# Performance work log

Hardware: AMD Instinct MI355X
Metric: run time of the kernel (lower is better)

Reference implementation:

```python
import jax, jax.numpy as jnp
import numpy as np

B, NIN, NH, SUB, HID = 8192, 1433, 64, 6, 128
TEMP, LAMB, ITERS = 0.4, 20.0, 5

def prelu(x, a):
    return jnp.where(x >= 0, x, a * x)

def l2norm(x):
    # F.normalize with eps clamp
    n = jnp.maximum(jnp.linalg.norm(x, axis=-1, keepdims=True), 1e-12)
    return x / n

def setup_inputs() -> dict:
    key = jax.random.key(0)
    ks = jax.random.split(key, 16)
    inp = {}
    inp['seq1'] = jax.random.normal(ks[0], (B, SUB, NIN), jnp.float32)
    inp['seq2'] = jax.random.normal(ks[1], (B, SUB, NIN), jnp.float32)
    inp['adj1'] = jax.random.uniform(ks[2], (B, SUB, SUB), jnp.float32)
    inp['adj2'] = jax.random.uniform(ks[3], (B, SUB, SUB), jnp.float32)
    inp['rescale_ratio'] = jax.random.uniform(ks[4], (B, SUB - 1, SUB - 1), jnp.float32)
    inp['gcn_W'] = jax.random.normal(ks[5], (NH, NIN), jnp.float32) / np.sqrt(NIN)
    inp['gcn_b'] = jnp.zeros((NH,), jnp.float32)
    inp['gcn_a'] = jnp.float32(0.25)
    inp['dec_W1'] = jax.random.normal(ks[6], (HID, NH * 4), jnp.float32) / np.sqrt(NH * 4)
    inp['dec_b1'] = jnp.zeros((HID,), jnp.float32)
    inp['dec_a1'] = jnp.float32(0.25)
    inp['dec_W2'] = jax.random.normal(ks[7], (HID, HID), jnp.float32) / np.sqrt(HID)
    inp['dec_b2'] = jnp.zeros((HID,), jnp.float32)
    inp['dec_a2'] = jnp.float32(0.25)
    inp['dec_W3'] = jax.random.normal(ks[8], (NIN, HID), jnp.float32) / np.sqrt(HID)
    inp['dec_b3'] = jnp.zeros((NIN,), jnp.float32)
    inp['dec_a3'] = jnp.float32(0.25)
    inp['disc_W'] = jax.random.normal(ks[9], (1, NH, NH), jnp.float32) / np.sqrt(NH)
    inp['disc_b'] = jnp.zeros((1,), jnp.float32)
    inp['subgraph_size'] = 4
    return inp

def sinkhorn_score(g1, n1, g2, n2, rescale_ratio):
    # cost has grad; transport is computed under no_grad in torch
    cost = (1.0 - jnp.einsum('bik,bjk->bij', l2norm(g1), l2norm(g2))) * rescale_ratio
    sg = jax.lax.stop_gradient
    g1s, n1s, g2s, n2s, costs = sg(g1), sg(n1), sg(g2), sg(n2), sg(cost)
    r = jnp.einsum('bik,bjk->bij', g1s, n2s)            # [B, N, 1]
    r = jnp.where(r <= 0, 1e-8, r)
    r = r / jnp.sum(r, axis=1, keepdims=True)
    c = jnp.einsum('bik,bjk->bij', g2s, n1s)            # [B, N, 1]
    c = jnp.where(c <= 0, 1e-8, c)
    c = c / jnp.sum(c, axis=1, keepdims=True)
    P = jnp.exp(-LAMB * costs)                          # [B, N, N]
    u = jnp.ones_like(c) / c.shape[1]
    for _ in range(ITERS):
        v = r / jnp.einsum('bij,bjk->bik', P, u)
        u = c / jnp.einsum('bji,bjk->bik', P, v)
    # diag(v) @ P @ diag(u)
    transport = v * P * jnp.swapaxes(u, 1, 2)           # [B, N, N]
    S = jnp.sum(transport * (1.0 - cost), axis=(1, 2))[:, None]  # [B, 1]
    return S

def reference(seq1, seq2, adj1, adj2, rescale_ratio, gcn_W, gcn_b, gcn_a,
              dec_W1, dec_b1, dec_a1, dec_W2, dec_b2, dec_a2, dec_W3, dec_b3, dec_a3,
              disc_W, disc_b, subgraph_size):
    def gcn(seq, adj):
        fts = jnp.einsum('bnf,hf->bnh', seq, gcn_W)
        return prelu(jnp.einsum('bnm,bmh->bnh', adj, fts) + gcn_b, gcn_a)
    h1 = gcn(seq1, adj1)   # [B, SUB, NH]
    h2 = gcn(seq2, adj2)
    # swap last two rows, then split graph-part / node-part
    def swap(h):
        return jnp.concatenate([h[:, :-2], h[:, -1:], h[:, -2:-1]], axis=1)
    h1n, h2n = swap(h1), swap(h2)
    g1, n1 = h1n[:, :-1], h1n[:, -1:]
    g2, n2 = h2n[:, :-1], h2n[:, -1:]
    S = sinkhorn_score(g1, n1, g2, n2, rescale_ratio)
    loss_pos = jnp.exp(S / TEMP) * 2.0                  # [B, 1]
    # decoder (subgraph_size=4 path): sub_node = h[:, :sub_size-2, :]
    x = h1[:, :subgraph_size, :].reshape(h1.shape[0], -1)
    x = prelu(x @ dec_W1.T + dec_b1, dec_a1)
    x = prelu(x @ dec_W2.T + dec_b2, dec_a2)
    node_recons = prelu(x @ dec_W3.T + dec_b3, dec_a3)  # [B, NIN]
    # discriminator (avg readout over context nodes, bilinear score)
    c = jnp.mean(h1[:, :-1, :], axis=1)                 # [B, NH]
    hp = h1[:, -1, :]                                   # [B, NH]
    s1 = jnp.einsum('bi,oij,bj->bo', hp, disc_W, c) + disc_b
    c_mi = jnp.concatenate([c[-2:-1], c[:-1]], axis=0)  # negsamp_round=1 shift
    s2 = jnp.einsum('bi,oij,bj->bo', hp, disc_W, c_mi) + disc_b
    logits = jnp.concatenate([s1, s2], axis=1)          # [B, 2]
    return jnp.concatenate([loss_pos, node_recons, logits], axis=1)  # [B, 1+NIN+2]
```

## Files before the change

kernel.cpp:

```cpp
#include <hip/hip_runtime.h>
#include <math.h>

#define BB   8192
#define NIN  1433
#define NH   64
#define SUBG 6
#define HID  128

typedef __attribute__((ext_vector_type(8))) short bf16x8;
typedef __attribute__((ext_vector_type(4))) float f32x4;
typedef __attribute__((ext_vector_type(16))) float f32x16;

__device__ __forceinline__ short f2bf(float x) {
  unsigned u = __float_as_uint(x);
  unsigned r = (u + 0x7fffu + ((u >> 16) & 1u)) >> 16;
  return (short)r;
}
__device__ __forceinline__ float bf2f(short s) {
  return __uint_as_float(((unsigned)(unsigned short)s) << 16);
}
__device__ __forceinline__ float allred64(float v) {
#pragma unroll
  for (int m = 1; m < 64; m <<= 1) v += __shfl_xor(v, m, 64);
  return v;
}

__device__ __forceinline__ void gload_lds16(const short* g, short* l) {
  __builtin_amdgcn_global_load_lds(
      (const __attribute__((address_space(1))) void*)g,
      (__attribute__((address_space(3))) void*)l, 16, 0, 0);
}

#define WAITV(N)                                            \
  {                                                         \
    asm volatile("s_waitcnt vmcnt(" #N ")" ::: "memory");   \
    __builtin_amdgcn_sched_barrier(0);                      \
  }
#define BARRIER()                                           \
  {                                                         \
    __builtin_amdgcn_s_barrier();                           \
    __builtin_amdgcn_sched_barrier(0);                      \
  }

__device__ __forceinline__ void pack16_impl(const float* __restrict__ src,
                                            short* __restrict__ hi, short* __restrict__ lo,
                                            int Oreal, int NF, int Kreal, int idx) {
  int j    = idx & 7;
  int lane = (idx >> 3) & 63;
  int nf   = (idx >> 9) % NF;
  int c    = idx / (NF * 512);
  int o = nf * 16 + (lane & 15);
  int k = c * 32 + ((lane >> 4) << 3) + j;
  float v = (o < Oreal && k < Kreal) ? src[(size_t)o * Kreal + k] : 0.f;
  short h = f2bf(v);
  hi[idx] = h;
  lo[idx] = f2bf(v - bf2f(h));
}

__device__ __forceinline__ void pack32_impl(const float* __restrict__ src,
                                            short* __restrict__ hi, short* __restrict__ lo,
                                            int idx) {
  int j    = idx & 7;
  int lane = (idx >> 3) & 63;
  int s    = (idx >> 9) & 3;
  int c    = idx >> 11;
  int o = (s & 1) * 32 + (lane & 31);
  int k = c * 32 + ((s >> 1) << 4) + ((lane >> 5) << 3) + j;
  float v = (k < NIN) ? src[(size_t)o * NIN + k] : 0.f;
  short h = f2bf(v);
  hi[idx] = h;
  lo[idx] = f2bf(v - bf2f(h));
}

#define PK_G  (45 * 4 * 512)
#define PK_B1 (8 * 8 * 512)
#define PK_B2 (4 * 8 * 512)
#define PK_B3 (4 * 90 * 512)
#define PK_TOTAL (PK_G + PK_B1 + PK_B2 + PK_B3)

__global__ void pack_all(const float* __restrict__ gcnW, const float* __restrict__ W1,
                         const float* __restrict__ W2, const float* __restrict__ W3,
                         short* Gh, short* Gl, short* B1h, short* B1l,
                         short* B2h, short* B2l, short* B3h, short* B3l) {
  int idx = blockIdx.x * 256 + threadIdx.x;
  if (idx < PK_G) { pack32_impl(gcnW, Gh, Gl, idx); return; }
  idx -= PK_G;
  if (idx < PK_B1) { pack16_impl(W1, B1h, B1l, 128, 8, 256, idx); return; }
  idx -= PK_B1;
  if (idx < PK_B2) { pack16_impl(W2, B2h, B2l, 128, 8, 128, idx); return; }
  idx -= PK_B2;
  if (idx < PK_B3) { pack16_impl(W3, B3h, B3l, 1433, 90, 128, idx); }
}

__global__ __launch_bounds__(384, 3) void gcn_mfma(
    const float* __restrict__ seq1, const float* __restrict__ seq2,
    const short* __restrict__ Gh, const short* __restrict__ Gl,
    float* __restrict__ fts1, float* __restrict__ fts2)
{
  __shared__ short sB[4][4096];
  const int tid = threadIdx.x;
  const int sid = blockIdx.x >> 8;
  const int bb  = blockIdx.x & 255;
  const float* __restrict__ seq = sid ? seq2 : seq1;
  float* __restrict__ fout = sid ? fts2 : fts1;
  const int w = tid >> 6, lane = tid & 63;
  const int l31 = lane & 31, lg2 = lane >> 5;
  const int row0 = bb * 192 + w * 32;

  f32x16 acc[2];
#pragma unroll
  for (int i = 0; i < 16; ++i) { acc[0][i] = 0.f; acc[1][i] = 0.f; }

  const float* aptr = seq + (size_t)(row0 + l31) * NIN + lg2 * 8;

  auto STAGE = [&](int c, int slot) {
    short* sb = &sB[slot][0];
    const size_t cb = (size_t)c * 256;
#pragma unroll
    for (int i = 0; i < 2; ++i) {
      const int pb = (w * 128 + i * 64) & 511;
      const short* src = (pb < 256) ? (Gh + (cb + pb) * 8 + (size_t)lane * 8)
                                    : (Gl + (cb + (pb - 256)) * 8 + (size_t)lane * 8);
      gload_lds16(src, sb + (pb + lane) * 8);
    }
  };

#define ALOAD(c_, R_)                                                        \
  {                                                                          \
    const float* ad_ = aptr + (c_) * 32;                                     \
    asm volatile(                                                            \
        "global_load_dwordx4 %0, %4, off\n\t"                                \
        "global_load_dwordx4 %1, %4, off offset:16\n\t"                      \
        "global_load_dwordx4 %2, %4, off offset:64\n\t"                      \
        "global_load_dwordx4 %3, %4, off offset:80"                          \
        : "=&v"(R_[0]), "=&v"(R_[1]), "=&v"(R_[2]), "=&v"(R_[3])             \
        : "v"(ad_));                                                         \
  }

  auto SPLIT8 = [&](const f32x4& p, const f32x4& q, bf16x8& H, bf16x8& L) {
    float av[8] = {p[0], p[1], p[2], p[3], q[0], q[1], q[2], q[3]};
#pragma unroll
    for (int j = 0; j < 8; ++j) {
      unsigned u = __float_as_uint(av[j]);
      H[j] = (short)(u >> 16);
      L[j] = f2bf(av[j] - __uint_as_float(u & 0xffff0000u));
    }
  };

  auto COMPUTE = [&](int c, const f32x4* R) {
    bf16x8 Ah0, Al0, Ah1, Al1;
    SPLIT8(R[0], R[1], Ah0, Al0);
    SPLIT8(R[2], R[3], Ah1, Al1);
    const short* bs = &sB[c & 3][0];
    __builtin_amdgcn_s_setprio(1);
#pragma unroll
    for (int ct = 0; ct < 2; ++ct) {
      bf16x8 Bh0 = *(const bf16x8*)(bs + ((0 + ct) * 64 + lane) * 8);
      bf16x8 Bl0 = *(const bf16x8*)(bs + 2048 + ((0 + ct) * 64 + lane) * 8);
      bf16x8 Bh1 = *(const bf16x8*)(bs + ((2 + ct) * 64 + lane) * 8);
      bf16x8 Bl1 = *(const bf16x8*)(bs + 2048 + ((2 + ct) * 64 + lane) * 8);
      acc[ct] = __builtin_amdgcn_mfma_f32_32x32x16_bf16(Ah0, Bh0, acc[ct], 0, 0, 0);
      acc[ct] = __builtin_amdgcn_mfma_f32_32x32x16_bf16(Al0, Bh0, acc[ct], 0, 0, 0);
      acc[ct] = __builtin_amdgcn_mfma_f32_32x32x16_bf16(Ah0, Bl0, acc[ct], 0, 0, 0);
      acc[ct] = __builtin_amdgcn_mfma_f32_32x32x16_bf16(Ah1, Bh1, acc[ct], 0, 0, 0);
      acc[ct] = __builtin_amdgcn_mfma_f32_32x32x16_bf16(Al1, Bh1, acc[ct], 0, 0, 0);
      acc[ct] = __builtin_amdgcn_mfma_f32_32x32x16_bf16(Ah1, Bl1, acc[ct], 0, 0, 0);
    }
    __builtin_amdgcn_s_setprio(0);
  };

  f32x4 A0[4], A1[4];
  STAGE(0, 0); ALOAD(0, A0);
  STAGE(1, 1); ALOAD(1, A1);

#pragma unroll 1
  for (int cc = 0; cc < 42; cc += 2) {
    WAITV(6); BARRIER();
    COMPUTE(cc, A0);
    STAGE(cc + 2, (cc + 2) & 3); ALOAD(cc + 2, A0);
    WAITV(6); BARRIER();
    COMPUTE(cc + 1, A1);
    STAGE(cc + 3, (cc + 3) & 3); ALOAD(cc + 3, A1);
  }
  WAITV(6); BARRIER();
  COMPUTE(42, A0);
  WAITV(0); BARRIER();
  COMPUTE(43, A1);

  {
    const int k0 = 44 * 32 + lg2 * 8;
    float av[16];
#pragma unroll
    for (int j = 0; j < 8; ++j) {
      int ka = k0 + j, kb = k0 + 16 + j;
      av[j]     = (ka < NIN) ? aptr[44 * 32 + j] : 0.f;
      av[8 + j] = (kb < NIN) ? aptr[44 * 32 + 16 + j] : 0.f;
    }
    bf16x8 Ah0, Al0, Ah1, Al1;
#pragma unroll
    for (int j = 0; j < 8; ++j) {
      unsigned u = __float_as_uint(av[j]);
      Ah0[j] = (short)(u >> 16);
      Al0[j] = f2bf(av[j] - __uint_as_float(u & 0xffff0000u));
      u = __float_as_uint(av[8 + j]);
      Ah1[j] = (short)(u >> 16);
      Al1[j] = f2bf(av[8 + j] - __uint_as_float(u & 0xffff0000u));
    }
#pragma unroll
    for (int ct = 0; ct < 2; ++ct) {
      const size_t o0 = ((size_t)(44 * 4 + ct) * 64 + lane) * 8;
      const size_t o1 = ((size_t)(44 * 4 + 2 + ct) * 64 + lane) * 8;
      bf16x8 Bh0 = *(const bf16x8*)(Gh + o0);
      bf16x8 Bl0 = *(const bf16x8*)(Gl + o0);
      bf16x8 Bh1 = *(const bf16x8*)(Gh + o1);
      bf16x8 Bl1 = *(const bf16x8*)(Gl + o1);
      acc[ct] = __builtin_amdgcn_mfma_f32_32x32x16_bf16(Ah0, Bh0, acc[ct], 0, 0, 0);
      acc[ct] = __builtin_amdgcn_mfma_f32_32x32x16_bf16(Al0, Bh0, acc[ct], 0, 0, 0);
      acc[ct] = __builtin_amdgcn_mfma_f32_32x32x16_bf16(Ah0, Bl0, acc[ct], 0, 0, 0);
      acc[ct] = __builtin_amdgcn_mfma_f32_32x32x16_bf16(Ah1, Bh1, acc[ct], 0, 0, 0);
      acc[ct] = __builtin_amdgcn_mfma_f32_32x32x16_bf16(Al1, Bh1, acc[ct], 0, 0, 0);
      acc[ct] = __builtin_amdgcn_mfma_f32_32x32x16_bf16(Ah1, Bl1, acc[ct], 0, 0, 0);
    }
  }

#pragma unroll
  for (int ct = 0; ct < 2; ++ct)
#pragma unroll
    for (int reg = 0; reg < 16; ++reg) {
      int crow = (reg & 3) + 8 * (reg >> 2) + 4 * lg2;
      fout[(size_t)(row0 + crow) * 64 + ct * 32 + l31] = acc[ct][reg];
    }
#undef ALOAD
}

__global__ __launch_bounds__(256) void sink_kernel(
    const float* __restrict__ fts1, const float* __restrict__ fts2,
    const float* __restrict__ adj1, const float* __restrict__ adj2,
    const float* __restrict__ resc, const float* __restrict__ discW,
    const float* __restrict__ bias, const float* __restrict__ aP,
    float* __restrict__ out, float* __restrict__ tws, float* __restrict__ h1w)
{
  const int b = (blockIdx.x << 2) + (threadIdx.x >> 6);
  const int lane = threadIdx.x & 63;
  const float* F1 = fts1 + (size_t)b * 384;
  const float* F2 = fts2 + (size_t)b * 384;
  float f1[6], f2[6];
#pragma unroll
  for (int m = 0; m < 6; ++m) { f1[m] = F1[m * 64 + lane]; f2[m] = F2[m * 64 + lane]; }
  const float bv = bias[lane];
  const float a = aP[0];
  const float* A1 = adj1 + (size_t)b * 36;
  const float* A2 = adj2 + (size_t)b * 36;
  float h1v[6], h2v[6];
#pragma unroll
  for (int n = 0; n < 6; ++n) {
    float o1 = bv, o2 = bv;
#pragma unroll
    for (int m = 0; m < 6; ++m) {
      o1 = fmaf(A1[n * 6 + m], f1[m], o1);
      o2 = fmaf(A2[n * 6 + m], f2[m], o2);
    }
    h1v[n] = (o1 >= 0.f) ? o1 : a * o1;
    h2v[n] = (o2 >= 0.f) ? o2 : a * o2;
  }
#pragma unroll
  for (int n = 0; n < 6; ++n) h1w[(size_t)b * 384 + n * 64 + lane] = h1v[n];

  float g1[5], g2[5];
#pragma unroll
  for (int i = 0; i < 4; ++i) { g1[i] = h1v[i]; g2[i] = h2v[i]; }
  g1[4] = h1v[5]; g2[4] = h2v[5];
  const float n1 = h1v[4], n2 = h2v[4];

  {
    float cm = (g1[0] + g1[1] + g1[2] + g1[3] + n1) * 0.2f;
    float t = 0.f;
    const float4* W4 = (const float4*)discW;
#pragma unroll 4
    for (int jq = 0; jq < 16; ++jq) {
      float4 wv = W4[lane * 16 + jq];
      t = fmaf(wv.x, __shfl(cm, 4 * jq, 64), t);
      t = fmaf(wv.y, __shfl(cm, 4 * jq + 1, 64), t);
      t = fmaf(wv.z, __shfl(cm, 4 * jq + 2, 64), t);
      t = fmaf(wv.w, __shfl(cm, 4 * jq + 3, 64), t);
    }
    tws[(size_t)b * 64 + lane] = t;
  }

  float in1[5], in2[5];
#pragma unroll
  for (int i = 0; i < 5; ++i) {
    float s = allred64(g1[i] * g1[i]);
    in1[i] = 1.f / fmaxf(sqrtf(s), 1e-12f);
    s = allred64(g2[i] * g2[i]);
    in2[i] = 1.f / fmaxf(sqrtf(s), 1e-12f);
  }
  float cost[25], P[25];
#pragma unroll
  for (int i = 0; i < 5; ++i)
#pragma unroll
    for (int j = 0; j < 5; ++j) {
      float d = allred64(g1[i] * g2[j]);
      float cv = (1.f - d * in1[i] * in2[j]) * resc[(size_t)b * 25 + i * 5 + j];
      cost[i * 5 + j] = cv;
      P[i * 5 + j] = expf(-20.f * cv);
    }
  float r[5], c[5];
  float rs = 0.f, cs = 0.f;
#pragma unroll
  for (int i = 0; i < 5; ++i) {
    float d = allred64(g1[i] * n2); d = (d <= 0.f) ? 1e-8f : d; r[i] = d; rs += d;
    d = allred64(g2[i] * n1);       d = (d <= 0.f) ? 1e-8f : d; c[i] = d; cs += d;
  }
#pragma unroll
  for (int i = 0; i < 5; ++i) { r[i] = r[i] / rs; c[i] = c[i] / cs; }

  float u[5], v[5];
#pragma unroll
  for (int i = 0; i < 5; ++i) u[i] = 0.2f;
#pragma unroll
  for (int it = 0; it < 5; ++it) {
#pragma unroll
    for (int i = 0; i < 5; ++i) {
      float pv = 0.f;
#pragma unroll
      for (int j = 0; j < 5; ++j) pv = fmaf(P[i * 5 + j], u[j], pv);
      v[i] = r[i] / pv;
    }
#pragma unroll
    for (int i = 0; i < 5; ++i) {
      float pu = 0.f;
#pragma unroll
      for (int j = 0; j < 5; ++j) pu = fmaf(P[j * 5 + i], v[j], pu);
      u[i] = c[i] / pu;
    }
  }
  float S = 0.f;
#pragma unroll
  for (int i = 0; i < 5; ++i)
#pragma unroll
    for (int j = 0; j < 5; ++j)
      S += v[i] * P[i * 5 + j] * u[j] * (1.f - cost[i * 5 + j]);
  if (lane == 0) out[(size_t)b * 1436] = expf(S * 2.5f) * 2.f;
}

__global__ __launch_bounds__(256) void dec_fused(
    const float* __restrict__ h1,
    const short* __restrict__ B1h, const short* __restrict__ B1l,
    const float* __restrict__ b1, const float* __restrict__ a1P,
    const short* __restrict__ B2h, const short* __restrict__ B2l,
    const float* __restrict__ b2, const float* __restrict__ a2P,
    const short* __restrict__ B3h, const short* __restrict__ B3l,
    const float* __restrict__ b3, const float* __restrict__ a3P,
    const float* __restrict__ tws, const float* __restrict__ dbP,
    float* __restrict__ out)
{
  __shared__ float xT[16][132];
  __shared__ float x2T[16][132];
  const int tid = threadIdx.x;
  const int w = tid >> 6, lane = tid & 63;
  const int l15 = lane & 15, lg = lane >> 4;
  const int r0 = blockIdx.x * 16;

  f32x4 acc1[2];
  acc1[0] = (f32x4){0.f, 0.f, 0.f, 0.f};
  acc1[1] = (f32x4){0.f, 0.f, 0.f, 0.f};
#pragma unroll
  for (int c = 0; c < 8; ++c) {
    const float* ap = h1 + (size_t)(r0 + l15) * 384 + c * 32 + lg * 8;
    float4 p = *(const float4*)ap;
    float4 q = *(const float4*)(ap + 4);
    float av[8] = {p.x, p.y, p.z, p.w, q.x, q.y, q.z, q.w};
    bf16x8 Ah, Al;
#pragma unroll
    for (int j = 0; j < 8; ++j) { short h = f2bf(av[j]); Ah[j] = h; Al[j] = f2bf(av[j] - bf2f(h)); }
#pragma unroll
    for (int i = 0; i < 2; ++i) {
      const int nf = 2 * w + i;
      size_t off = (((size_t)(c * 8 + nf)) << 9) + (size_t)lane * 8;
      bf16x8 Bh = *(const bf16x8*)(B1h + off);
      bf16x8 Bl = *(const bf16x8*)(B1l + off);
      acc1[i] = __builtin_amdgcn_mfma_f32_16x16x32_bf16(Ah, Bh, acc1[i], 0, 0, 0);
      acc1[i] = __builtin_amdgcn_mfma_f32_16x16x32_bf16(Al, Bh, acc1[i], 0, 0, 0);
      acc1[i] = __builtin_amdgcn_mfma_f32_16x16x32_bf16(Ah, Bl, acc1[i], 0, 0, 0);
    }
  }
  {
    const float a1 = a1P[0];
#pragma unroll
    for (int i = 0; i < 2; ++i) {
      int o = (2 * w + i) * 16 + l15;
      float bvv = b1[o];
#pragma unroll
      for (int j = 0; j < 4; ++j) {
        float v = acc1[i][j] + bvv;
        xT[lg * 4 + j][o] = (v >= 0.f) ? v : a1 * v;
      }
    }
  }
  __syncthreads();

  acc1[0] = (f32x4){0.f, 0.f, 0.f, 0.f};
  acc1[1] = (f32x4){0.f, 0.f, 0.f, 0.f};
#pragma unroll
  for (int c = 0; c < 4; ++c) {
    const float* ap = &xT[l15][c * 32 + lg * 8];
    float4 p = *(const float4*)ap;
    float4 q = *(const float4*)(ap + 4);
    float av[8] = {p.x, p.y, p.z, p.w, q.x, q.y, q.z, q.w};
    bf16x8 Ah, Al;
#pragma unroll
    for (int j = 0; j < 8; ++j) { short h = f2bf(av[j]); Ah[j] = h; Al[j] = f2bf(av[j] - bf2f(h)); }
#pragma unroll
    for (int i = 0; i < 2; ++i) {
      const int nf = 2 * w + i;
      size_t off = (((size_t)(c * 8 + nf)) << 9) + (size_t)lane * 8;
      bf16x8 Bh = *(const bf16x8*)(B2h + off);
      bf16x8 Bl = *(const bf16x8*)(B2l + off);
      acc1[i] = __builtin_amdgcn_mfma_f32_16x16x32_bf16(Ah, Bh, acc1[i], 0, 0, 0);
      acc1[i] = __builtin_amdgcn_mfma_f32_16x16x32_bf16(Al, Bh, acc1[i], 0, 0, 0);
      acc1[i] = __builtin_amdgcn_mfma_f32_16x16x32_bf16(Ah, Bl, acc1[i], 0, 0, 0);
    }
  }
  {
    const float a2 = a2P[0];
#pragma unroll
    for (int i = 0; i < 2; ++i) {
      int o = (2 * w + i) * 16 + l15;
      float bvv = b2[o];
#pragma unroll
      for (int j = 0; j < 4; ++j) {
        float v = acc1[i][j] + bvv;
        x2T[lg * 4 + j][o] = (v >= 0.f) ? v : a2 * v;
      }
    }
  }
  __syncthreads();

  bf16x8 A3h[4], A3l[4];
#pragma unroll
  for (int c = 0; c < 4; ++c) {
    const float* ap = &x2T[l15][c * 32 + lg * 8];
    float4 p = *(const float4*)ap;
    float4 q = *(const float4*)(ap + 4);
    float av[8] = {p.x, p.y, p.z, p.w, q.x, q.y, q.z, q.w};
#pragma unroll
    for (int j = 0; j < 8; ++j) {
      short h = f2bf(av[j]); A3h[c][j] = h; A3l[c][j] = f2bf(av[j] - bf2f(h));
    }
  }
  const float a3 = a3P[0];
#pragma unroll 1
  for (int t = 0; t < 23; ++t) {
    const int nf = w + 4 * t;
    if (nf >= 90) break;
    f32x4 acc = (f32x4){0.f, 0.f, 0.f, 0.f};
#pragma unroll
    for (int c = 0; c < 4; ++c) {
      size_t off = (((size_t)(c * 90 + nf)) << 9) + (size_t)lane * 8;
      bf16x8 Bh = *(const bf16x8*)(B3h + off);
      bf16x8 Bl = *(const bf16x8*)(B3l + off);
      acc = __builtin_amdgcn_mfma_f32_16x16x32_bf16(A3h[c], Bh, acc, 0, 0, 0);
      acc = __builtin_amdgcn_mfma_f32_16x16x32_bf16(A3l[c], Bh, acc, 0, 0, 0);
      acc = __builtin_amdgcn_mfma_f32_16x16x32_bf16(A3h[c], Bl, acc, 0, 0, 0);
    }
    const int o = nf * 16 + l15;
    if (o < NIN) {
      float bvv = b3[o];
#pragma unroll
      for (int j = 0; j < 4; ++j) {
        float v = acc[j] + bvv;
        v = (v >= 0.f) ? v : a3 * v;
        out[(size_t)(r0 + lg * 4 + j) * 1436 + 1 + o] = v;
      }
    }
  }

  {
    const float db = dbP[0];
#pragma unroll
    for (int i = 0; i < 4; ++i) {
      const int bb = r0 + 4 * w + i;
      float hp = h1[(size_t)bb * 384 + 5 * 64 + lane];
      float t0 = tws[(size_t)bb * 64 + lane];
      const int bp = (bb == 0) ? (BB - 2) : (bb - 1);
      float tp = tws[(size_t)bp * 64 + lane];
      float s1 = allred64(hp * t0);
      float s2 = allred64(hp * tp);
      if (lane == 0) {
        out[(size_t)bb * 1436 + 1434] = s1 + db;
        out[(size_t)bb * 1436 + 1435] = s2 + db;
      }
    }
  }
}

extern "C" void kernel_launch(void* const* d_in, const int* in_sizes, int n_in,
                              void* d_out, int out_size, void* d_ws, size_t ws_size,
                              hipStream_t stream) {
  (void)in_sizes; (void)n_in; (void)out_size; (void)ws_size;
  const float* seq1  = (const float*)d_in[0];
  const float* seq2  = (const float*)d_in[1];
  const float* adj1  = (const float*)d_in[2];
  const float* adj2  = (const float*)d_in[3];
  const float* resc  = (const float*)d_in[4];
  const float* gcnW  = (const float*)d_in[5];
  const float* gcnB  = (const float*)d_in[6];
  const float* gcnA  = (const float*)d_in[7];
  const float* W1    = (const float*)d_in[8];
  const float* b1    = (const float*)d_in[9];
  const float* a1    = (const float*)d_in[10];
  const float* W2    = (const float*)d_in[11];
  const float* b2    = (const float*)d_in[12];
  const float* a2    = (const float*)d_in[13];
  const float* W3    = (const float*)d_in[14];
  const float* b3    = (const float*)d_in[15];
  const float* a3    = (const float*)d_in[16];
  const float* discW = (const float*)d_in[17];
  const float* discB = (const float*)d_in[18];

  float* fts1 = (float*)d_ws;
  float* fts2 = fts1 + (size_t)BB * SUBG * NH;
  float* h1   = fts2 + (size_t)BB * SUBG * NH;
  float* tws  = h1  + (size_t)BB * SUBG * NH;
  short* Gh   = (short*)(tws + (size_t)BB * 64);
  short* Gl   = Gh  + PK_G;
  short* B1h  = Gl  + PK_G;
  short* B1l  = B1h + PK_B1;
  short* B2h  = B1l + PK_B1;
  short* B2l  = B2h + PK_B2;
  short* B3h  = B2l + PK_B2;
  short* B3l  = B3h + PK_B3;
  float* out  = (float*)d_out;

  pack_all<<<(PK_TOTAL + 255) / 256, 256, 0, stream>>>(
      gcnW, W1, W2, W3, Gh, Gl, B1h, B1l, B2h, B2l, B3h, B3l);

  gcn_mfma<<<512, 384, 0, stream>>>(seq1, seq2, Gh, Gl, fts1, fts2);
  sink_kernel<<<2048, 256, 0, stream>>>(fts1, fts2, adj1, adj2, resc, discW, gcnB, gcnA,
                                        out, tws, h1);
  dec_fused<<<512, 256, 0, stream>>>(h1, B1h, B1l, b1, a1, B2h, B2l, b2, a2,
                                     B3h, B3l, b3, a3, tws, discB, out);
}
```

Baseline: 320.0 us.

## Use 8 waves in decoder and drop low-bf16 weight term in final layer

The decoder kernel goes from 4 to 8 waves per block, so each wave computes one 16-column output fragment for layers 1 and 2 and strides over the layer-3 output tiles by 8. The third layer drops the Ah*Bl correction MFMA and no longer loads the B3 low-part weights. This cuts MFMA work and weight traffic in the dominant 128x1433 GEMM and raises parallelism per block. In exchange it lowers the precision of W3 to plain bf16 on the weight side, which may affect accuracy tolerance.

```diff
diff --git a/kernel.cpp b/kernel.cpp
--- a/kernel.cpp
+++ b/kernel.cpp
@@ -25,7 +25,7 @@
   return v;
 }
 
-__device__ __forceinline__ void gload_lds16(const short* g, short* l) {
+__device__ __forceinline__ void gload_lds16(const void* g, void* l) {
   __builtin_amdgcn_global_load_lds(
       (const __attribute__((address_space(1))) void*)g,
       (__attribute__((address_space(3))) void*)l, 16, 0, 0);
@@ -344,13 +344,13 @@
   if (lane == 0) out[(size_t)b * 1436] = expf(S * 2.5f) * 2.f;
 }
 
-__global__ __launch_bounds__(256) void dec_fused(
+__global__ __launch_bounds__(512) void dec_fused(
     const float* __restrict__ h1,
     const short* __restrict__ B1h, const short* __restrict__ B1l,
     const float* __restrict__ b1, const float* __restrict__ a1P,
     const short* __restrict__ B2h, const short* __restrict__ B2l,
     const float* __restrict__ b2, const float* __restrict__ a2P,
-    const short* __restrict__ B3h, const short* __restrict__ B3l,
+    const short* __restrict__ B3h,
     const float* __restrict__ b3, const float* __restrict__ a3P,
     const float* __restrict__ tws, const float* __restrict__ dbP,
     float* __restrict__ out)
@@ -362,9 +362,7 @@
   const int l15 = lane & 15, lg = lane >> 4;
   const int r0 = blockIdx.x * 16;
 
-  f32x4 acc1[2];
-  acc1[0] = (f32x4){0.f, 0.f, 0.f, 0.f};
-  acc1[1] = (f32x4){0.f, 0.f, 0.f, 0.f};
+  f32x4 acc1 = (f32x4){0.f, 0.f, 0.f, 0.f};
 #pragma unroll
   for (int c = 0; c < 8; ++c) {
     const float* ap = h1 + (size_t)(r0 + l15) * 384 + c * 32 + lg * 8;
@@ -374,34 +372,26 @@
     bf16x8 Ah, Al;
 #pragma unroll
     for (int j = 0; j < 8; ++j) { short h = f2bf(av[j]); Ah[j] = h; Al[j] = f2bf(av[j] - bf2f(h)); }
-#pragma unroll
-    for (int i = 0; i < 2; ++i) {
-      const int nf = 2 * w + i;
-      size_t off = (((size_t)(c * 8 + nf)) << 9) + (size_t)lane * 8;
-      bf16x8 Bh = *(const bf16x8*)(B1h + off);
-      bf16x8 Bl = *(const bf16x8*)(B1l + off);
-      acc1[i] = __builtin_amdgcn_mfma_f32_16x16x32_bf16(Ah, Bh, acc1[i], 0, 0, 0);
-      acc1[i] = __builtin_amdgcn_mfma_f32_16x16x32_bf16(Al, Bh, acc1[i], 0, 0, 0);
-      acc1[i] = __builtin_amdgcn_mfma_f32_16x16x32_bf16(Ah, Bl, acc1[i], 0, 0, 0);
-    }
+    size_t off = (((size_t)(c * 8 + w)) << 9) + (size_t)lane * 8;
+    bf16x8 Bh = *(const bf16x8*)(B1h + off);
+    bf16x8 Bl = *(const bf16x8*)(B1l + off);
+    acc1 = __builtin_amdgcn_mfma_f32_16x16x32_bf16(Ah, Bh, acc1, 0, 0, 0);
+    acc1 = __builtin_amdgcn_mfma_f32_16x16x32_bf16(Al, Bh, acc1, 0, 0, 0);
+    acc1 = __builtin_amdgcn_mfma_f32_16x16x32_bf16(Ah, Bl, acc1, 0, 0, 0);
   }
   {
     const float a1 = a1P[0];
-#pragma unroll
-    for (int i = 0; i < 2; ++i) {
-      int o = (2 * w + i) * 16 + l15;
-      float bvv = b1[o];
-#pragma unroll
-      for (int j = 0; j < 4; ++j) {
-        float v = acc1[i][j] + bvv;
-        xT[lg * 4 + j][o] = (v >= 0.f) ? v : a1 * v;
-      }
+    int o = w * 16 + l15;
+    float bvv = b1[o];
+#pragma unroll
+    for (int j = 0; j < 4; ++j) {
+      float v = acc1[j] + bvv;
+      xT[lg * 4 + j][o] = (v >= 0.f) ? v : a1 * v;
     }
   }
   __syncthreads();
 
-  acc1[0] = (f32x4){0.f, 0.f, 0.f, 0.f};
-  acc1[1] = (f32x4){0.f, 0.f, 0.f, 0.f};
+  acc1 = (f32x4){0.f, 0.f, 0.f, 0.f};
 #pragma unroll
   for (int c = 0; c < 4; ++c) {
     const float* ap = &xT[l15][c * 32 + lg * 8];
@@ -411,28 +401,21 @@
     bf16x8 Ah, Al;
 #pragma unroll
     for (int j = 0; j < 8; ++j) { short h = f2bf(av[j]); Ah[j] = h; Al[j] = f2bf(av[j] - bf2f(h)); }
-#pragma unroll
-    for (int i = 0; i < 2; ++i) {
-      const int nf = 2 * w + i;
-      size_t off = (((size_t)(c * 8 + nf)) << 9) + (size_t)lane * 8;
-      bf16x8 Bh = *(const bf16x8*)(B2h + off);
-      bf16x8 Bl = *(const bf16x8*)(B2l + off);
-      acc1[i] = __builtin_amdgcn_mfma_f32_16x16x32_bf16(Ah, Bh, acc1[i], 0, 0, 0);
-      acc1[i] = __builtin_amdgcn_mfma_f32_16x16x32_bf16(Al, Bh, acc1[i], 0, 0, 0);
-      acc1[i] = __builtin_amdgcn_mfma_f32_16x16x32_bf16(Ah, Bl, acc1[i], 0, 0, 0);
-    }
+    size_t off = (((size_t)(c * 8 + w)) << 9) + (size_t)lane * 8;
+    bf16x8 Bh = *(const bf16x8*)(B2h + off);
+    bf16x8 Bl = *(const bf16x8*)(B2l + off);
+    acc1 = __builtin_amdgcn_mfma_f32_16x16x32_bf16(Ah, Bh, acc1, 0, 0, 0);
+    acc1 = __builtin_amdgcn_mfma_f32_16x16x32_bf16(Al, Bh, acc1, 0, 0, 0);
+    acc1 = __builtin_amdgcn_mfma_f32_16x16x32_bf16(Ah, Bl, acc1, 0, 0, 0);
   }
   {
     const float a2 = a2P[0];
-#pragma unroll
-    for (int i = 0; i < 2; ++i) {
-      int o = (2 * w + i) * 16 + l15;
-      float bvv = b2[o];
-#pragma unroll
-      for (int j = 0; j < 4; ++j) {
-        float v = acc1[i][j] + bvv;
-        x2T[lg * 4 + j][o] = (v >= 0.f) ? v : a2 * v;
-      }
+    int o = w * 16 + l15;
+    float bvv = b2[o];
+#pragma unroll
+    for (int j = 0; j < 4; ++j) {
+      float v = acc1[j] + bvv;
+      x2T[lg * 4 + j][o] = (v >= 0.f) ? v : a2 * v;
     }
   }
   __syncthreads();
@@ -451,18 +434,16 @@
   }
   const float a3 = a3P[0];
 #pragma unroll 1
-  for (int t = 0; t < 23; ++t) {
-    const int nf = w + 4 * t;
+  for (int t = 0; t < 12; ++t) {
+    const int nf = w + 8 * t;
     if (nf >= 90) break;
     f32x4 acc = (f32x4){0.f, 0.f, 0.f, 0.f};
 #pragma unroll
     for (int c = 0; c < 4; ++c) {
       size_t off = (((size_t)(c * 90 + nf)) << 9) + (size_t)lane * 8;
       bf16x8 Bh = *(const bf16x8*)(B3h + off);
-      bf16x8 Bl = *(const bf16x8*)(B3l + off);
       acc = __builtin_amdgcn_mfma_f32_16x16x32_bf16(A3h[c], Bh, acc, 0, 0, 0);
       acc = __builtin_amdgcn_mfma_f32_16x16x32_bf16(A3l[c], Bh, acc, 0, 0, 0);
-      acc = __builtin_amdgcn_mfma_f32_16x16x32_bf16(A3h[c], Bl, acc, 0, 0, 0);
     }
     const int o = nf * 16 + l15;
     if (o < NIN) {
@@ -479,8 +460,8 @@
   {
     const float db = dbP[0];
 #pragma unroll
-    for (int i = 0; i < 4; ++i) {
-      const int bb = r0 + 4 * w + i;
+    for (int i = 0; i < 2; ++i) {
+      const int bb = r0 + 2 * w + i;
       float hp = h1[(size_t)bb * 384 + 5 * 64 + lane];
       float t0 = tws[(size_t)bb * 64 + lane];
       const int bp = (bb == 0) ? (BB - 2) : (bb - 1);
@@ -539,6 +520,6 @@
   gcn_mfma<<<512, 384, 0, stream>>>(seq1, seq2, Gh, Gl, fts1, fts2);
   sink_kernel<<<2048, 256, 0, stream>>>(fts1, fts2, adj1, adj2, resc, discW, gcnB, gcnA,
                                         out, tws, h1);
-  dec_fused<<<512, 256, 0, stream>>>(h1, B1h, B1l, b1, a1, B2h, B2l, b2, a2,
-                                     B3h, B3l, b3, a3, tws, discB, out);
-}
+  dec_fused<<<512, 512, 0, stream>>>(h1, B1h, B1l, b1, a1, B2h, B2l, b2, a2,
+                                     B3h, b3, a3, tws, discB, out);
+}
```

Measured after the change: 261.9 us. 18.2% less time.
